# Kernel optimization log

Measured on AMD Instinct MI355X. Metric: run time of the kernel, lower is better.

Reference implementation:

```python
import jax, jax.numpy as jnp
import numpy as np

CODEBOOK_SIZE = 16384
CODEBOOK_DIM = 14   # log2(CODEBOOK_SIZE)
NUM_CODEBOOKS = 1
TEMPERATURE = 0.01
EPS = 1e-5
SAMPLE_MIN_W = 1.0
BATCH_MAX_W = 1.0


def _make_codebook(dtype):
    # big-endian bits of all codes, mapped to {-1, +1}; shape [K, D]
    codes = jnp.arange(CODEBOOK_SIZE)
    mask = 2 ** jnp.arange(CODEBOOK_DIM)
    bits = ((codes[:, None] & mask[None, :]) != 0).astype(dtype)
    return bits * 2.0 - 1.0


def setup_inputs() -> dict:
    key = jax.random.key(0)
    x = jax.random.normal(key, (8, 1024, NUM_CODEBOOKS * CODEBOOK_DIM), dtype=jnp.float32)
    return {"x": x}


def reference(x):
    b, l, c = x.shape
    xr = x.reshape(b, l, NUM_CODEBOOKS, CODEBOOK_DIM)  # b n c d

    # sign-threshold quantization
    quantized = jnp.where(xr > 0, jnp.asarray(1.0, x.dtype), jnp.asarray(-1.0, x.dtype))

    # training path: logits against full codebook + entropy loss
    codebook = _make_codebook(x.dtype)                 # [K, D]
    logits = 2.0 * jnp.einsum('bncd,jd->bncj', xr, codebook)  # [b,n,c,K]
    s = logits / TEMPERATURE
    probs = jax.nn.softmax(s, axis=-1)
    log_probs = jax.nn.log_softmax(s + EPS, axis=-1)   # +eps matches torch source
    avg_probs = probs.mean(axis=(0, 1, 2))             # '... D -> D' mean
    avg_entropy = -jnp.sum(avg_probs * jnp.log(avg_probs + EPS))
    sample_entropy = jnp.mean(-jnp.sum(probs * log_probs, axis=-1))
    entropy_aux_loss = SAMPLE_MIN_W * sample_entropy - BATCH_MAX_W * avg_entropy

    # commitment loss (quantized is detached in torch; fwd value identical)
    commit_loss = jnp.mean((xr - quantized) ** 2)

    # straight-through estimator (fwd value == quantized)
    q_st = xr + jax.lax.stop_gradient(quantized - xr)
    q_out = q_st.reshape(b, l, c)

    return q_out, entropy_aux_loss, sample_entropy, avg_entropy, commit_loss
```

## Files before the change

kernel.cpp:

```cpp
#include <hip/hip_runtime.h>


#define N_SAMPLES 8192
#define DIMS      14
#define KCODES    16384
#define LFQ_EPS   1e-5f

__global__ void __launch_bounds__(256)
lfq_main(const float* __restrict__ x,
         float* __restrict__ qout,
         float* __restrict__ avgp,
         float* __restrict__ acc)
{
    const int i = blockIdx.x * 256 + threadIdx.x;
    float commit = 0.f, sampH = 0.f;

    const float* xp = x + (size_t)i * DIMS;
    float* qp = qout + (size_t)i * DIMS;

    int code = 0;
    float sumLog = 0.f;
    int   softd[DIMS];
    float softt[DIMS];
    int   S = 0;

#pragma unroll
    for (int d = 0; d < DIMS; ++d) {
        float xv = xp[d];
        bool pos = xv > 0.f;
        float q = pos ? 1.f : -1.f;
        qp[d] = q;
        float diff = xv - q;
        commit += diff * diff;
        code |= (pos ? 1 : 0) << d;

        float v = 400.f * fabsf(xv);
        float t = __expf(-v);
        float l1p = log1pf(t);
        sumLog += l1p;
        sampH += l1p + v * t / (1.f + t);
        if (t > 1e-7f) { softd[S] = d; softt[S] = t; ++S; }
    }

    float base = __expf(-sumLog);
    int nsub = 1 << S;
    for (int m = 0; m < nsub; ++m) {
        float mass = base;
        int c = code;
        for (int k = 0; k < S; ++k) {
            if ((m >> k) & 1) { mass *= softt[k]; c ^= 1 << softd[k]; }
        }
        if (mass > 1e-12f) atomicAdd(&avgp[c], mass);
    }

    for (int off = 32; off > 0; off >>= 1) {
        commit += __shfl_down(commit, off);
        sampH  += __shfl_down(sampH,  off);
    }
    if ((threadIdx.x & 63) == 0) {
        atomicAdd(&acc[0], commit);
        atomicAdd(&acc[1], sampH);
    }
}

__global__ void __launch_bounds__(256)
lfq_final(const float* __restrict__ avgp,
          const float* __restrict__ acc,
          float* __restrict__ out)
{
    __shared__ float red[256];
    float e = 0.f;
    for (int j = threadIdx.x; j < KCODES; j += 256) {
        float a = avgp[j] * (1.f / (float)N_SAMPLES);
        e -= a * logf(a + LFQ_EPS);
    }
    red[threadIdx.x] = e;
    __syncthreads();
    for (int s = 128; s > 0; s >>= 1) {
        if (threadIdx.x < s) red[threadIdx.x] += red[threadIdx.x + s];
        __syncthreads();
    }
    if (threadIdx.x == 0) {
        float avgH    = red[0];
        float sampleH = acc[1] * (1.f / (float)N_SAMPLES);
        float commit  = acc[0] * (1.f / (float)(N_SAMPLES * DIMS));
        float aux     = sampleH - avgH;
        out[N_SAMPLES * DIMS + 0] = aux;
        out[N_SAMPLES * DIMS + 1] = sampleH;
        out[N_SAMPLES * DIMS + 2] = avgH;
        out[N_SAMPLES * DIMS + 3] = commit;
    }
}

extern "C" void kernel_launch(void* const* d_in, const int* in_sizes, int n_in,
                              void* d_out, int out_size, void* d_ws, size_t ws_size,
                              hipStream_t stream) {
    const float* x = (const float*)d_in[0];
    float* out = (float*)d_out;
    float* avgp = (float*)d_ws;
    float* acc  = avgp + KCODES;

    hipMemsetAsync(d_ws, 0, (KCODES + 2) * sizeof(float), stream);
    lfq_main<<<N_SAMPLES / 256, 256, 0, stream>>>(x, out, avgp, acc);
    lfq_final<<<1, 256, 0, stream>>>(avgp, acc, out);
}
```

Measured before the change: 86.24 us.

## Fuse memset, main and final kernels into one cooperative kernel with grid syncs

Replaces the memset, the main kernel and the single-block final reduction with one cooperative kernel of 32 blocks. The workspace is zeroed in-kernel, then grid.sync separates accumulation, a distributed entropy reduction over the 16384 codes, and the final scalar writes. This removes two launches and the serial single-block reduction, in exchange for three grid-wide barriers and the overhead of a cooperative launch.

Result: slower. 97.47 us (+13.0%).

```diff
diff --git a/kernel.cpp b/kernel.cpp
--- a/kernel.cpp
+++ b/kernel.cpp
@@ -1,20 +1,30 @@
 #include <hip/hip_runtime.h>
+#include <hip/hip_cooperative_groups.h>
+
+namespace cg = cooperative_groups;
 
 
 #define N_SAMPLES 8192
 #define DIMS      14
 #define KCODES    16384
 #define LFQ_EPS   1e-5f
+#define NBLOCKS   (N_SAMPLES / 256)
 
 __global__ void __launch_bounds__(256)
-lfq_main(const float* __restrict__ x,
-         float* __restrict__ qout,
-         float* __restrict__ avgp,
-         float* __restrict__ acc)
+lfq_fused(const float* __restrict__ x,
+          float* __restrict__ qout,
+          float* __restrict__ avgp,
+          float* __restrict__ acc)
 {
+    cg::grid_group grid = cg::this_grid();
     const int i = blockIdx.x * 256 + threadIdx.x;
+
+    avgp[2 * i]     = 0.f;
+    avgp[2 * i + 1] = 0.f;
+    if (i < 3) acc[i] = 0.f;
+    grid.sync();
+
     float commit = 0.f, sampH = 0.f;
-
     const float* xp = x + (size_t)i * DIMS;
     float* qp = qout + (size_t)i * DIMS;
 
@@ -61,34 +71,28 @@
         atomicAdd(&acc[0], commit);
         atomicAdd(&acc[1], sampH);
     }
-}
+    grid.sync();
 
-__global__ void __launch_bounds__(256)
-lfq_final(const float* __restrict__ avgp,
-          const float* __restrict__ acc,
-          float* __restrict__ out)
-{
-    __shared__ float red[256];
-    float e = 0.f;
-    for (int j = threadIdx.x; j < KCODES; j += 256) {
-        float a = avgp[j] * (1.f / (float)N_SAMPLES);
-        e -= a * logf(a + LFQ_EPS);
+    {
+        float a0 = avgp[2 * i]     * (1.f / (float)N_SAMPLES);
+        float a1 = avgp[2 * i + 1] * (1.f / (float)N_SAMPLES);
+        float e = -a0 * logf(a0 + LFQ_EPS) - a1 * logf(a1 + LFQ_EPS);
+        for (int off = 32; off > 0; off >>= 1)
+            e += __shfl_down(e, off);
+        if ((threadIdx.x & 63) == 0)
+            atomicAdd(&acc[2], e);
     }
-    red[threadIdx.x] = e;
-    __syncthreads();
-    for (int s = 128; s > 0; s >>= 1) {
-        if (threadIdx.x < s) red[threadIdx.x] += red[threadIdx.x + s];
-        __syncthreads();
-    }
-    if (threadIdx.x == 0) {
-        float avgH    = red[0];
+    grid.sync();
+
+    if (i == 0) {
+        float avgH    = acc[2];
         float sampleH = acc[1] * (1.f / (float)N_SAMPLES);
-        float commit  = acc[0] * (1.f / (float)(N_SAMPLES * DIMS));
+        float commitL = acc[0] * (1.f / (float)(N_SAMPLES * DIMS));
         float aux     = sampleH - avgH;
-        out[N_SAMPLES * DIMS + 0] = aux;
-        out[N_SAMPLES * DIMS + 1] = sampleH;
-        out[N_SAMPLES * DIMS + 2] = avgH;
-        out[N_SAMPLES * DIMS + 3] = commit;
+        qout[N_SAMPLES * DIMS + 0] = aux;
+        qout[N_SAMPLES * DIMS + 1] = sampleH;
+        qout[N_SAMPLES * DIMS + 2] = avgH;
+        qout[N_SAMPLES * DIMS + 3] = commitL;
     }
 }
 
@@ -96,11 +100,11 @@
                               void* d_out, int out_size, void* d_ws, size_t ws_size,
                               hipStream_t stream) {
     const float* x = (const float*)d_in[0];
-    float* out = (float*)d_out;
+    float* out  = (float*)d_out;
     float* avgp = (float*)d_ws;
     float* acc  = avgp + KCODES;
 
-    hipMemsetAsync(d_ws, 0, (KCODES + 2) * sizeof(float), stream);
-    lfq_main<<<N_SAMPLES / 256, 256, 0, stream>>>(x, out, avgp, acc);
-    lfq_final<<<1, 256, 0, stream>>>(avgp, acc, out);
+    void* args[] = { (void*)&x, (void*)&out, (void*)&avgp, (void*)&acc };
+    hipLaunchCooperativeKernel((const void*)lfq_fused,
+                               dim3(NBLOCKS), dim3(256), args, 0, stream);
 }
```
